# Kernel tuning notes

Measured on AMD Instinct MI355X. Metric: run time of the kernel, lower is better.

The kernel has to match this reference:

```python
import jax, jax.numpy as jnp
import numpy as np

B, S, H, K = 64, 512, 1024, 7

def setup_inputs() -> dict:
    key = jax.random.key(0)
    ks = jax.random.split(key, 7)
    x = jax.random.normal(ks[0], (B, S, H), dtype=jnp.float32)
    gt = jax.random.randint(ks[1], (B, S), 0, K, dtype=jnp.int64)
    mask = jnp.ones((B, S), dtype=bool)
    # learned parameters
    W = jax.random.normal(ks[2], (H, K), dtype=jnp.float32) * (1.0 / np.sqrt(H))
    b = jnp.zeros((K,), dtype=jnp.float32)
    start_trans = jax.random.uniform(ks[3], (K,), minval=-0.1, maxval=0.1)
    end_trans = jax.random.uniform(ks[4], (K,), minval=-0.1, maxval=0.1)
    trans = jax.random.uniform(ks[5], (K, K), minval=-0.1, maxval=0.1)
    return {"x": x, "gt": gt, "mask": mask, "W": W, "b": b,
            "start_trans": start_trans, "end_trans": end_trans, "trans": trans}

def _crf_neg_llh(emissions, gt, mask, start_trans, end_trans, trans):
    # emissions: [B,S,K], gt: [B,S] int, mask: [B,S] bool
    maskf = mask.astype(emissions.dtype)
    # ---- numerator: score of gold path ----
    em_at_tag = jnp.take_along_axis(emissions, gt[..., None], axis=-1)[..., 0]  # [B,S]
    trans_sc = trans[gt[:, :-1], gt[:, 1:]]                                      # [B,S-1]
    num = start_trans[gt[:, 0]] + em_at_tag[:, 0]
    num = num + jnp.sum((trans_sc + em_at_tag[:, 1:]) * maskf[:, 1:], axis=1)
    last_idx = jnp.sum(mask, axis=1).astype(jnp.int32) - 1                       # [B]
    last_tags = jnp.take_along_axis(gt, last_idx[:, None], axis=1)[:, 0]
    num = num + end_trans[last_tags]
    # ---- denominator: log partition via forward algorithm (lax.scan) ----
    alpha0 = start_trans[None, :] + emissions[:, 0]                              # [B,K]
    em_rest = jnp.transpose(emissions[:, 1:], (1, 0, 2))                         # [S-1,B,K]
    m_rest = jnp.transpose(mask[:, 1:], (1, 0))                                  # [S-1,B]
    def step(alpha, inp):
        em_t, m_t = inp
        nxt = jax.nn.logsumexp(alpha[:, :, None] + trans[None, :, :] + em_t[:, None, :], axis=1)
        return jnp.where(m_t[:, None], nxt, alpha), None
    alpha, _ = jax.lax.scan(step, alpha0, (em_rest, m_rest))
    denom = jax.nn.logsumexp(alpha + end_trans[None, :], axis=1)                 # [B]
    llh = num - denom
    return -jnp.mean(llh)  # reduction='mean', module returns negative

def reference(x, gt, mask, W, b, start_trans, end_trans, trans):
    emissions = jnp.einsum('bsh,hk->bsk', x, W) + b
    return _crf_neg_llh(emissions, gt, mask, start_trans, end_trans, trans)
```

## Files before the change

kernel.cpp:

```cpp
#include <hip/hip_runtime.h>
#include <math.h>

#define NB 64
#define NS 512
#define NH 1024
#define NK 7
#define NCHUNK 16
#define CLEN 32

#define WS_ALPHA0  0
#define WS_NUMP    (WS_ALPHA0 + 64 * 8)
#define WS_CHUNKP  (WS_NUMP + 64 * 16)

typedef float f32x4 __attribute__((ext_vector_type(4)));

template <int CTRL>
__device__ __forceinline__ float dpp_add(float v) {
    const int sh = __builtin_amdgcn_update_dpp(0, __float_as_int(v),
                                               CTRL, 0xF, 0xF, true);
    return v + __int_as_float(sh);
}
template <int PAT>
__device__ __forceinline__ float swz_add(float v) {
    const int sh = __builtin_amdgcn_ds_swizzle(__float_as_int(v), PAT);
    return v + __int_as_float(sh);
}

__device__ __forceinline__ void emit_rows(
    const float* __restrict__ x, size_t row0, int q, int g, int lane,
    const float (&wlin)[28], float (*lds_q)[4][9])
{
#define WV(i, k) wlin[(i) * 7 + (k)]
    const float4* xq = (const float4*)(x + row0 * NH) + q * 64 + lane;
    float4 xb[4];
#pragma unroll
    for (int j = 0; j < 4; ++j)
        xb[j] = xq[(size_t)(g + 2 * j) * (NH / 4)];
#pragma unroll
    for (int j = 0; j < 16; ++j) {
        const float4 v = xb[j & 3];
        if (j + 4 < 16)
            xb[j & 3] = xq[(size_t)(g + 2 * (j + 4)) * (NH / 4)];
        float acc[NK];
#pragma unroll
        for (int k = 0; k < NK; ++k)
            acc[k] = v.x * WV(0, k) + v.y * WV(1, k)
                   + v.z * WV(2, k) + v.w * WV(3, k);
#pragma unroll
        for (int k = 0; k < NK; ++k) {
            acc[k] = dpp_add<0xB1>(acc[k]);
            acc[k] = dpp_add<0x4E>(acc[k]);
            acc[k] = dpp_add<0x141>(acc[k]);
        }
        const int ss = lane & 7;
        const float v01 = (ss & 1) ? acc[1] : acc[0];
        const float v23 = (ss & 1) ? acc[3] : acc[2];
        const float v45 = (ss & 1) ? acc[5] : acc[4];
        const float w03 = (ss & 2) ? v23 : v01;
        const float w47 = (ss & 2) ? acc[6] : v45;
        float r8 = (ss & 4) ? w47 : w03;
        r8 = swz_add<0x201F>(r8);
        r8 = swz_add<0x401F>(r8);
        r8 += __shfl_xor(r8, 32, 64);
        if (lane < NK) lds_q[g + 2 * j][q][lane] = r8;
    }
#undef WV
}

__device__ __forceinline__ void num_partial(
    const int* __restrict__ gt32, const float* __restrict__ st,
    const float* __restrict__ et, const float* lds_tr, const float* lem,
    int b, int ch, int lane, float* __restrict__ numP)
{
    int oddbits = 0;
    for (int i = lane; i < 256; i += 64) oddbits |= gt32[2 * i + 1];
    const bool is64 = (__ballot(oddbits != 0) == 0ull);
    const int tloc = lane & 31;
    const int tg = ch * CLEN + tloc;
    const int gidx = b * NS + tg;
    const int g2 = is64 ? gt32[2 * gidx] : gt32[gidx];
    float term = 0.f;
    if (lane < 32) {
        if (tg == 0) {
            term = st[g2] + lem[g2];
        } else {
            const int pidx = gidx - 1;
            const int gp = is64 ? gt32[2 * pidx] : gt32[pidx];
            term = lds_tr[gp * 7 + g2] + lem[tloc * 8 + g2];
        }
        if (tg == NS - 1) term += et[g2];
    }
#pragma unroll
    for (int m = 1; m < 64; m <<= 1) term += __shfl_xor(term, m, 64);
    if (lane == 0) numP[b * NCHUNK + ch] = term;
}

__device__ __forceinline__ void scan_chunk(
    const float* lds_tr, const float* lem, int b, int ch, int lane,
    float* __restrict__ chunkP)
{
    const int li = lane < 49 ? lane : 48;
    const int i = li / 7;
    const int k = li - i * 7;
    float tj[NK];
#pragma unroll
    for (int j = 0; j < NK; ++j) tj[j] = lds_tr[j * 7 + k];
    const int first = (ch == 0) ? 1 : 0;
    float P = lds_tr[i * 7 + k] + lem[first * 8 + k];
    for (int t = first + 1; t < CLEN; ++t) {
        float a[NK];
#pragma unroll
        for (int j = 0; j < NK; ++j)
            a[j] = __shfl(P, i * 7 + j, 64) + tj[j];
        const float m = fmaxf(fmaxf(fmaxf(a[0], a[1]), fmaxf(a[2], a[3])),
                              fmaxf(fmaxf(a[4], a[5]), a[6]));
        const float su = __expf(a[0]-m) + __expf(a[1]-m) + __expf(a[2]-m)
                       + __expf(a[3]-m) + __expf(a[4]-m) + __expf(a[5]-m)
                       + __expf(a[6]-m);
        P = m + __logf(su) + lem[t * 8 + k];
    }
    if (lane < 49)
        chunkP[(size_t)(b * NCHUNK + ch) * 49 + lane] = P;
}

__global__ __launch_bounds__(512) void fused_emis_chunk(
    const float* __restrict__ x, const float* __restrict__ W,
    const float* __restrict__ bias, const float* __restrict__ trans,
    const float* __restrict__ start_trans, const float* __restrict__ end_trans,
    const int* __restrict__ gt32, float* __restrict__ ws)
{
    __shared__ float lds_q[CLEN][4][9];
    __shared__ float lds_em[2][CLEN * 8];
    __shared__ float lds_tr[49];

    float* __restrict__ alpha0g = ws + WS_ALPHA0;
    float* __restrict__ numP    = ws + WS_NUMP;
    float* __restrict__ chunkP  = ws + WS_CHUNKP;

    const int tid  = threadIdx.x;
    const int lane = tid & 63;
    const int wave = tid >> 6;
    const int q    = wave & 3;
    const int g    = wave >> 2;
    const int b  = blockIdx.x >> 3;
    const int cc = blockIdx.x & 7;
    const int cA = 2 * cc;
    const int cB = 2 * cc + 1;
    const size_t row0A = (size_t)b * NS + cA * CLEN;
    const size_t row0B = (size_t)b * NS + cB * CLEN;

    if (tid < 49) lds_tr[tid] = trans[tid];

    f32x4 wf0, wf1, wf2, wf3, wf4, wf5, wf6;
    {
        const float* wbase = W + (size_t)28 * (q * 64 + lane);
        asm volatile("global_load_dwordx4 %0, %1, off"            : "=v"(wf0) : "v"(wbase));
        asm volatile("global_load_dwordx4 %0, %1, off offset:16"  : "=v"(wf1) : "v"(wbase));
        asm volatile("global_load_dwordx4 %0, %1, off offset:32"  : "=v"(wf2) : "v"(wbase));
        asm volatile("global_load_dwordx4 %0, %1, off offset:48"  : "=v"(wf3) : "v"(wbase));
        asm volatile("global_load_dwordx4 %0, %1, off offset:64"  : "=v"(wf4) : "v"(wbase));
        asm volatile("global_load_dwordx4 %0, %1, off offset:80"  : "=v"(wf5) : "v"(wbase));
        asm volatile("global_load_dwordx4 %0, %1, off offset:96"  : "=v"(wf6) : "v"(wbase));
        asm volatile("s_waitcnt vmcnt(0)"
                     : "+v"(wf0), "+v"(wf1), "+v"(wf2), "+v"(wf3),
                       "+v"(wf4), "+v"(wf5), "+v"(wf6));
    }
    float wlin[28];
#pragma unroll
    for (int e = 0; e < 4; ++e) {
        wlin[e]      = wf0[e]; wlin[4 + e]  = wf1[e]; wlin[8 + e]  = wf2[e];
        wlin[12 + e] = wf3[e]; wlin[16 + e] = wf4[e]; wlin[20 + e] = wf5[e];
        wlin[24 + e] = wf6[e];
    }

    emit_rows(x, row0A, q, g, lane, wlin, lds_q);
    __syncthreads();

    if (tid < CLEN * NK) {
        const int r = tid / NK;
        const int k = tid - r * NK;
        lds_em[0][r * 8 + k] = lds_q[r][0][k] + lds_q[r][1][k]
                             + lds_q[r][2][k] + lds_q[r][3][k] + bias[k];
    }
    __syncthreads();

    if (wave == 0) {
        if (cc == 0 && lane < NK)
            alpha0g[b * 8 + lane] = start_trans[lane] + lds_em[0][lane];
        num_partial(gt32, start_trans, end_trans, lds_tr, lds_em[0],
                    b, cA, lane, numP);
        scan_chunk(lds_tr, lds_em[0], b, cA, lane, chunkP);
    }
    emit_rows(x, row0B, q, g, lane, wlin, lds_q);
    __syncthreads();

    if (tid < CLEN * NK) {
        const int r = tid / NK;
        const int k = tid - r * NK;
        lds_em[1][r * 8 + k] = lds_q[r][0][k] + lds_q[r][1][k]
                             + lds_q[r][2][k] + lds_q[r][3][k] + bias[k];
    }
    __syncthreads();

    if (wave == 1) {
        num_partial(gt32, start_trans, end_trans, lds_tr, lds_em[1],
                    b, cB, lane, numP);
        scan_chunk(lds_tr, lds_em[1], b, cB, lane, chunkP);
    }
}

__global__ __launch_bounds__(64) void combine_kernel(
    const float* __restrict__ ws, const float* __restrict__ end_trans,
    float* __restrict__ out)
{
    __shared__ float lds_C[NCHUNK * 49];
    const float* __restrict__ alpha0g = ws + WS_ALPHA0;
    const float* __restrict__ numP    = ws + WS_NUMP;
    const float* __restrict__ chunkP  = ws + WS_CHUNKP;
    const int b    = blockIdx.x;
    const int lane = threadIdx.x;

    for (int idx = lane; idx < NCHUNK * 49; idx += 64)
        lds_C[idx] = chunkP[(size_t)b * NCHUNK * 49 + idx];
    __syncthreads();

    float np = (lane < NCHUNK) ? numP[b * NCHUNK + lane] : 0.f;
#pragma unroll
    for (int m = 1; m < 16; m <<= 1) np += __shfl_xor(np, m, 64);
    const float num = __shfl(np, 0, 64);

    const int kk = lane < NK ? lane : NK - 1;
    float alpha = alpha0g[b * 8 + kk];
#pragma unroll
    for (int c = 0; c < NCHUNK; ++c) {
        float a[NK];
#pragma unroll
        for (int j = 0; j < NK; ++j)
            a[j] = __shfl(alpha, j, 64) + lds_C[c * 49 + j * 7 + kk];
        const float m = fmaxf(fmaxf(fmaxf(a[0], a[1]), fmaxf(a[2], a[3])),
                              fmaxf(fmaxf(a[4], a[5]), a[6]));
        const float su = __expf(a[0]-m) + __expf(a[1]-m) + __expf(a[2]-m)
                       + __expf(a[3]-m) + __expf(a[4]-m) + __expf(a[5]-m)
                       + __expf(a[6]-m);
        alpha = m + __logf(su);
    }

    float v = (lane < NK) ? (alpha + end_trans[kk]) : -3.0e38f;
    float mv = v;
#pragma unroll
    for (int m = 1; m < 8; m <<= 1) mv = fmaxf(mv, __shfl_xor(mv, m, 64));
    float e = (lane < NK) ? __expf(v - mv) : 0.f;
#pragma unroll
    for (int m = 1; m < 8; m <<= 1) e += __shfl_xor(e, m, 64);
    if (lane == 0)
        atomicAdd(out, ((mv + __logf(e)) - num) * (1.0f / NB));
}

extern "C" void kernel_launch(void* const* d_in, const int* in_sizes, int n_in,
                              void* d_out, int out_size, void* d_ws, size_t ws_size,
                              hipStream_t stream)
{
    const float* x    = (const float*)d_in[0];
    const int*   gt   = (const int*)d_in[1];
    const float* W    = (const float*)d_in[3];
    const float* bias = (const float*)d_in[4];
    const float* st   = (const float*)d_in[5];
    const float* et   = (const float*)d_in[6];
    const float* tr   = (const float*)d_in[7];

    float* ws = (float*)d_ws;

    (void)hipMemsetAsync(d_out, 0, sizeof(float) * out_size, stream);
    fused_emis_chunk<<<NB * (NCHUNK / 2), 512, 0, stream>>>(
        x, W, bias, tr, st, et, gt, ws);
    combine_kernel<<<NB, 64, 0, stream>>>(ws, et, (float*)d_out);
}
```

Before: 228.1 us.

## Use one chunk per block with an 8-deep asm load ring for x rows

Each block now handles a single 32-row chunk, so the grid doubles to 1024 blocks, and the old two-chunk in-block overlap of scan with the next chunk's emission is dropped. The x loads now go through an 8-entry register ring built from inline-asm global_load_dwordx4 with explicit vmcnt waits, keeping more loads in flight. The aim is more memory-level parallelism and more blocks in flight on a bandwidth-bound GEMV. The cost is that W is reloaded for every chunk, and the serial scan on wave 0 now runs while the other waves sit idle or exit.

```diff
diff --git a/kernel.cpp b/kernel.cpp
--- a/kernel.cpp
+++ b/kernel.cpp
@@ -26,101 +26,48 @@
     return v + __int_as_float(sh);
 }
 
-__device__ __forceinline__ void emit_rows(
-    const float* __restrict__ x, size_t row0, int q, int g, int lane,
-    const float (&wlin)[28], float (*lds_q)[4][9])
+__device__ __forceinline__ void gload16(f32x4& d, const float* p) {
+    asm volatile("global_load_dwordx4 %0, %1, off" : "=v"(d) : "v"(p));
+}
+template <int N>
+__device__ __forceinline__ void wait_vmcnt(f32x4& v) {
+    if      constexpr (N == 7) asm volatile("s_waitcnt vmcnt(7)" : "+v"(v));
+    else if constexpr (N == 6) asm volatile("s_waitcnt vmcnt(6)" : "+v"(v));
+    else if constexpr (N == 5) asm volatile("s_waitcnt vmcnt(5)" : "+v"(v));
+    else if constexpr (N == 4) asm volatile("s_waitcnt vmcnt(4)" : "+v"(v));
+    else if constexpr (N == 3) asm volatile("s_waitcnt vmcnt(3)" : "+v"(v));
+    else if constexpr (N == 2) asm volatile("s_waitcnt vmcnt(2)" : "+v"(v));
+    else if constexpr (N == 1) asm volatile("s_waitcnt vmcnt(1)" : "+v"(v));
+    else                       asm volatile("s_waitcnt vmcnt(0)" : "+v"(v));
+}
+
+__device__ __forceinline__ void reduce_store(
+    const f32x4 v, const float (&wlin)[28], int lane, float* dst7)
 {
 #define WV(i, k) wlin[(i) * 7 + (k)]
-    const float4* xq = (const float4*)(x + row0 * NH) + q * 64 + lane;
-    float4 xb[4];
-#pragma unroll
-    for (int j = 0; j < 4; ++j)
-        xb[j] = xq[(size_t)(g + 2 * j) * (NH / 4)];
-#pragma unroll
-    for (int j = 0; j < 16; ++j) {
-        const float4 v = xb[j & 3];
-        if (j + 4 < 16)
-            xb[j & 3] = xq[(size_t)(g + 2 * (j + 4)) * (NH / 4)];
-        float acc[NK];
-#pragma unroll
-        for (int k = 0; k < NK; ++k)
-            acc[k] = v.x * WV(0, k) + v.y * WV(1, k)
-                   + v.z * WV(2, k) + v.w * WV(3, k);
-#pragma unroll
-        for (int k = 0; k < NK; ++k) {
-            acc[k] = dpp_add<0xB1>(acc[k]);
-            acc[k] = dpp_add<0x4E>(acc[k]);
-            acc[k] = dpp_add<0x141>(acc[k]);
-        }
-        const int ss = lane & 7;
-        const float v01 = (ss & 1) ? acc[1] : acc[0];
-        const float v23 = (ss & 1) ? acc[3] : acc[2];
-        const float v45 = (ss & 1) ? acc[5] : acc[4];
-        const float w03 = (ss & 2) ? v23 : v01;
-        const float w47 = (ss & 2) ? acc[6] : v45;
-        float r8 = (ss & 4) ? w47 : w03;
-        r8 = swz_add<0x201F>(r8);
-        r8 = swz_add<0x401F>(r8);
-        r8 += __shfl_xor(r8, 32, 64);
-        if (lane < NK) lds_q[g + 2 * j][q][lane] = r8;
-    }
+    float acc[NK];
+#pragma unroll
+    for (int k = 0; k < NK; ++k)
+        acc[k] = v.x * WV(0, k) + v.y * WV(1, k)
+               + v.z * WV(2, k) + v.w * WV(3, k);
+#pragma unroll
+    for (int k = 0; k < NK; ++k) {
+        acc[k] = dpp_add<0xB1>(acc[k]);
+        acc[k] = dpp_add<0x4E>(acc[k]);
+        acc[k] = dpp_add<0x141>(acc[k]);
+    }
+    const int ss = lane & 7;
+    const float v01 = (ss & 1) ? acc[1] : acc[0];
+    const float v23 = (ss & 1) ? acc[3] : acc[2];
+    const float v45 = (ss & 1) ? acc[5] : acc[4];
+    const float w03 = (ss & 2) ? v23 : v01;
+    const float w47 = (ss & 2) ? acc[6] : v45;
+    float r8 = (ss & 4) ? w47 : w03;
+    r8 = swz_add<0x201F>(r8);
+    r8 = swz_add<0x401F>(r8);
+    r8 += __shfl_xor(r8, 32, 64);
+    if (lane < NK) dst7[lane] = r8;
 #undef WV
-}
-
-__device__ __forceinline__ void num_partial(
-    const int* __restrict__ gt32, const float* __restrict__ st,
-    const float* __restrict__ et, const float* lds_tr, const float* lem,
-    int b, int ch, int lane, float* __restrict__ numP)
-{
-    int oddbits = 0;
-    for (int i = lane; i < 256; i += 64) oddbits |= gt32[2 * i + 1];
-    const bool is64 = (__ballot(oddbits != 0) == 0ull);
-    const int tloc = lane & 31;
-    const int tg = ch * CLEN + tloc;
-    const int gidx = b * NS + tg;
-    const int g2 = is64 ? gt32[2 * gidx] : gt32[gidx];
-    float term = 0.f;
-    if (lane < 32) {
-        if (tg == 0) {
-            term = st[g2] + lem[g2];
-        } else {
-            const int pidx = gidx - 1;
-            const int gp = is64 ? gt32[2 * pidx] : gt32[pidx];
-            term = lds_tr[gp * 7 + g2] + lem[tloc * 8 + g2];
-        }
-        if (tg == NS - 1) term += et[g2];
-    }
-#pragma unroll
-    for (int m = 1; m < 64; m <<= 1) term += __shfl_xor(term, m, 64);
-    if (lane == 0) numP[b * NCHUNK + ch] = term;
-}
-
-__device__ __forceinline__ void scan_chunk(
-    const float* lds_tr, const float* lem, int b, int ch, int lane,
-    float* __restrict__ chunkP)
-{
-    const int li = lane < 49 ? lane : 48;
-    const int i = li / 7;
-    const int k = li - i * 7;
-    float tj[NK];
-#pragma unroll
-    for (int j = 0; j < NK; ++j) tj[j] = lds_tr[j * 7 + k];
-    const int first = (ch == 0) ? 1 : 0;
-    float P = lds_tr[i * 7 + k] + lem[first * 8 + k];
-    for (int t = first + 1; t < CLEN; ++t) {
-        float a[NK];
-#pragma unroll
-        for (int j = 0; j < NK; ++j)
-            a[j] = __shfl(P, i * 7 + j, 64) + tj[j];
-        const float m = fmaxf(fmaxf(fmaxf(a[0], a[1]), fmaxf(a[2], a[3])),
-                              fmaxf(fmaxf(a[4], a[5]), a[6]));
-        const float su = __expf(a[0]-m) + __expf(a[1]-m) + __expf(a[2]-m)
-                       + __expf(a[3]-m) + __expf(a[4]-m) + __expf(a[5]-m)
-                       + __expf(a[6]-m);
-        P = m + __logf(su) + lem[t * 8 + k];
-    }
-    if (lane < 49)
-        chunkP[(size_t)(b * NCHUNK + ch) * 49 + lane] = P;
 }
 
 __global__ __launch_bounds__(512) void fused_emis_chunk(
@@ -130,7 +77,7 @@
     const int* __restrict__ gt32, float* __restrict__ ws)
 {
     __shared__ float lds_q[CLEN][4][9];
-    __shared__ float lds_em[2][CLEN * 8];
+    __shared__ float lds_em[CLEN * 8];
     __shared__ float lds_tr[49];
 
     float* __restrict__ alpha0g = ws + WS_ALPHA0;
@@ -142,25 +89,22 @@
     const int wave = tid >> 6;
     const int q    = wave & 3;
     const int g    = wave >> 2;
-    const int b  = blockIdx.x >> 3;
-    const int cc = blockIdx.x & 7;
-    const int cA = 2 * cc;
-    const int cB = 2 * cc + 1;
-    const size_t row0A = (size_t)b * NS + cA * CLEN;
-    const size_t row0B = (size_t)b * NS + cB * CLEN;
+    const int b = blockIdx.x >> 4;
+    const int c = blockIdx.x & (NCHUNK - 1);
+    const size_t row0 = (size_t)b * NS + c * CLEN;
 
     if (tid < 49) lds_tr[tid] = trans[tid];
 
     f32x4 wf0, wf1, wf2, wf3, wf4, wf5, wf6;
     {
         const float* wbase = W + (size_t)28 * (q * 64 + lane);
-        asm volatile("global_load_dwordx4 %0, %1, off"            : "=v"(wf0) : "v"(wbase));
-        asm volatile("global_load_dwordx4 %0, %1, off offset:16"  : "=v"(wf1) : "v"(wbase));
-        asm volatile("global_load_dwordx4 %0, %1, off offset:32"  : "=v"(wf2) : "v"(wbase));
-        asm volatile("global_load_dwordx4 %0, %1, off offset:48"  : "=v"(wf3) : "v"(wbase));
-        asm volatile("global_load_dwordx4 %0, %1, off offset:64"  : "=v"(wf4) : "v"(wbase));
-        asm volatile("global_load_dwordx4 %0, %1, off offset:80"  : "=v"(wf5) : "v"(wbase));
-        asm volatile("global_load_dwordx4 %0, %1, off offset:96"  : "=v"(wf6) : "v"(wbase));
+        gload16(wf0, wbase);
+        gload16(wf1, wbase + 4);
+        gload16(wf2, wbase + 8);
+        gload16(wf3, wbase + 12);
+        gload16(wf4, wbase + 16);
+        gload16(wf5, wbase + 20);
+        gload16(wf6, wbase + 24);
         asm volatile("s_waitcnt vmcnt(0)"
                      : "+v"(wf0), "+v"(wf1), "+v"(wf2), "+v"(wf3),
                        "+v"(wf4), "+v"(wf5), "+v"(wf6));
@@ -173,39 +117,88 @@
         wlin[24 + e] = wf6[e];
     }
 
-    emit_rows(x, row0A, q, g, lane, wlin, lds_q);
+    __builtin_amdgcn_sched_barrier(0);
+    const float* xrow = x + row0 * NH + (size_t)(q * 64 + lane) * 4;
+    f32x4 rb[8];
+#pragma unroll
+    for (int j = 0; j < 8; ++j)
+        gload16(rb[j], xrow + (size_t)(g + 2 * j) * NH);
+
+#define RING_STEP(J)                                                         \
+    {                                                                        \
+        wait_vmcnt<((J) <= 8 ? 7 : 15 - (J))>(rb[(J) & 7]);                  \
+        const f32x4 vx = rb[(J) & 7];                                        \
+        if ((J) + 8 < 16)                                                    \
+            gload16(rb[(J) & 7], xrow + (size_t)(g + 2 * ((J) + 8)) * NH);   \
+        reduce_store(vx, wlin, lane, &lds_q[g + 2 * (J)][q][0]);             \
+    }
+    RING_STEP(0)  RING_STEP(1)  RING_STEP(2)  RING_STEP(3)
+    RING_STEP(4)  RING_STEP(5)  RING_STEP(6)  RING_STEP(7)
+    RING_STEP(8)  RING_STEP(9)  RING_STEP(10) RING_STEP(11)
+    RING_STEP(12) RING_STEP(13) RING_STEP(14) RING_STEP(15)
+#undef RING_STEP
+    __builtin_amdgcn_sched_barrier(0);
     __syncthreads();
 
     if (tid < CLEN * NK) {
         const int r = tid / NK;
         const int k = tid - r * NK;
-        lds_em[0][r * 8 + k] = lds_q[r][0][k] + lds_q[r][1][k]
-                             + lds_q[r][2][k] + lds_q[r][3][k] + bias[k];
+        lds_em[r * 8 + k] = lds_q[r][0][k] + lds_q[r][1][k]
+                          + lds_q[r][2][k] + lds_q[r][3][k] + bias[k];
     }
     __syncthreads();
-
-    if (wave == 0) {
-        if (cc == 0 && lane < NK)
-            alpha0g[b * 8 + lane] = start_trans[lane] + lds_em[0][lane];
-        num_partial(gt32, start_trans, end_trans, lds_tr, lds_em[0],
-                    b, cA, lane, numP);
-        scan_chunk(lds_tr, lds_em[0], b, cA, lane, chunkP);
-    }
-    emit_rows(x, row0B, q, g, lane, wlin, lds_q);
-    __syncthreads();
-
-    if (tid < CLEN * NK) {
-        const int r = tid / NK;
-        const int k = tid - r * NK;
-        lds_em[1][r * 8 + k] = lds_q[r][0][k] + lds_q[r][1][k]
-                             + lds_q[r][2][k] + lds_q[r][3][k] + bias[k];
-    }
-    __syncthreads();
-
-    if (wave == 1) {
-        num_partial(gt32, start_trans, end_trans, lds_tr, lds_em[1],
-                    b, cB, lane, numP);
-        scan_chunk(lds_tr, lds_em[1], b, cB, lane, chunkP);
+    if (wave != 0) return;
+
+    if (c == 0 && lane < NK)
+        alpha0g[b * 8 + lane] = start_trans[lane] + lds_em[lane];
+
+    {
+        int oddbits = 0;
+        for (int i = lane; i < 256; i += 64) oddbits |= gt32[2 * i + 1];
+        const bool is64 = (__ballot(oddbits != 0) == 0ull);
+        const int tloc = lane & 31;
+        const int tg = c * CLEN + tloc;
+        const int gidx = b * NS + tg;
+        const int g2 = is64 ? gt32[2 * gidx] : gt32[gidx];
+        float term = 0.f;
+        if (lane < 32) {
+            if (tg == 0) {
+                term = start_trans[g2] + lds_em[g2];
+            } else {
+                const int pidx = gidx - 1;
+                const int gp = is64 ? gt32[2 * pidx] : gt32[pidx];
+                term = lds_tr[gp * 7 + g2] + lds_em[tloc * 8 + g2];
+            }
+            if (tg == NS - 1) term += end_trans[g2];
+        }
+#pragma unroll
+        for (int m = 1; m < 64; m <<= 1) term += __shfl_xor(term, m, 64);
+        if (lane == 0) numP[b * NCHUNK + c] = term;
+    }
+
+    {
+        const int li = lane < 49 ? lane : 48;
+        const int i = li / 7;
+        const int k = li - i * 7;
+        float tj[NK];
+#pragma unroll
+        for (int j = 0; j < NK; ++j) tj[j] = lds_tr[j * 7 + k];
+        const int first = (c == 0) ? 1 : 0;
+        float P = lds_tr[i * 7 + k] + lds_em[first * 8 + k];
+        for (int t = first + 1; t < CLEN; ++t) {
+            float a[NK];
+#pragma unroll
+            for (int j = 0; j < NK; ++j)
+                a[j] = __shfl(P, i * 7 + j, 64) + tj[j];
+            const float m = fmaxf(fmaxf(fmaxf(a[0], a[1]), fmaxf(a[2], a[3])),
+                                  fmaxf(fmaxf(a[4], a[5]), a[6]));
+            const float su = __expf(a[0]-m) + __expf(a[1]-m) + __expf(a[2]-m)
+                           + __expf(a[3]-m) + __expf(a[4]-m) + __expf(a[5]-m)
+                           + __expf(a[6]-m);
+            P = m + __logf(su) + lds_em[t * 8 + k];
+        }
+        if (lane < 49)
+            chunkP[(size_t)(b * NCHUNK + c) * 49 + lane] = P;
     }
 }
 
@@ -271,7 +264,7 @@
     float* ws = (float*)d_ws;
 
     (void)hipMemsetAsync(d_out, 0, sizeof(float) * out_size, stream);
-    fused_emis_chunk<<<NB * (NCHUNK / 2), 512, 0, stream>>>(
+    fused_emis_chunk<<<NB * NCHUNK, 512, 0, stream>>>(
         x, W, bias, tr, st, et, gt, ws);
     combine_kernel<<<NB, 64, 0, stream>>>(ws, et, (float*)d_out);
 }
```

Measured after the change: 223.2 us. 2.2% less time.
